# Kernel optimization log

Hardware: AMD Instinct MI355X
Metric: run time of the kernel (lower is better)

## Reference

```python
import jax, jax.numpy as jnp
import numpy as np

N_NODES = 100000
N_EDGES = 3200000
D_IN = 256
D_OUT = 256


def setup_inputs() -> dict:
    key = jax.random.key(0)
    k1, k2, k3, k4, k5 = jax.random.split(key, 5)
    inputs = jax.random.normal(k1, (N_NODES, D_IN), dtype=jnp.float32)
    # Glorot-uniform init as in _glorot_init
    init_range = np.sqrt(6.0 / (D_IN + D_OUT)).astype(np.float32)
    weight = jax.random.uniform(k2, (D_IN, D_OUT), dtype=jnp.float32,
                                minval=-init_range, maxval=init_range)
    edge_src = jax.random.randint(k3, (N_EDGES,), 0, N_NODES, dtype=jnp.int32)
    edge_dst = jax.random.randint(k4, (N_EDGES,), 0, N_NODES, dtype=jnp.int32)
    # normalized adjacency values (positive, like D^-1/2 A D^-1/2 entries)
    edge_vals = jax.random.uniform(k5, (N_EDGES,), dtype=jnp.float32)
    return {"inputs": inputs, "weight": weight, "edge_src": edge_src,
            "edge_dst": edge_dst, "edge_vals": edge_vals}


def reference(inputs, weight, edge_src, edge_dst, edge_vals):
    # x = inputs @ W          : [N, D_OUT]
    x = inputs @ weight
    # SpMM: out[d] = sum_{e: dst(e)=d} vals[e] * x[src(e)]
    msgs = edge_vals[:, None] * x[edge_src]          # [E, D_OUT]
    out = jax.ops.segment_sum(msgs, edge_dst, num_segments=inputs.shape[0])
    return jax.nn.relu(out)
```

## Files before the change

### kernel.cpp

```cpp
#include <hip/hip_runtime.h>

#define N_NODES 100000
#define N_EDGES 3200000
#define DDIM 256
#define NB 1563
#define BIN_BLK 256
#define CHUNK (N_EDGES / BIN_BLK)
#define TB 1024

typedef short s16x8 __attribute__((ext_vector_type(8)));
typedef float f32x4 __attribute__((ext_vector_type(4)));
typedef float f32x2 __attribute__((ext_vector_type(2)));

__device__ __forceinline__ unsigned short f32_to_bf16(float f) {
    union { float f; unsigned int u; } c; c.f = f;
    unsigned int u = c.u;
    unsigned int r = u + 0x7fffu + ((u >> 16) & 1u);
    return (unsigned short)(r >> 16);
}
__device__ __forceinline__ float bl16(unsigned int u) {
    union { unsigned int x; float f; } c; c.x = u << 16; return c.f;
}
__device__ __forceinline__ float bh16(unsigned int u) {
    union { unsigned int x; float f; } c; c.x = u & 0xffff0000u; return c.f;
}

__global__ __launch_bounds__(256) void prep_w(const float* __restrict__ W,
                                              unsigned short* __restrict__ Wt) {
    __shared__ float tile[32][33];
    const int tx = threadIdx.x & 31;
    const int ty = threadIdx.x >> 5;
    const int n0 = blockIdx.x * 32;
    const int k0 = blockIdx.y * 32;
    for (int i = 0; i < 32; i += 8)
        tile[ty + i][tx] = W[(size_t)(k0 + ty + i) * DDIM + n0 + tx];
    __syncthreads();
    for (int i = 0; i < 32; i += 8)
        Wt[(size_t)(n0 + ty + i) * DDIM + k0 + tx] = f32_to_bf16(tile[tx][ty + i]);
}

__global__ __launch_bounds__(256) void gemm_mfma(const float* __restrict__ A,
                                                 const unsigned short* __restrict__ Wt,
                                                 unsigned short* __restrict__ Xb) {
    __shared__ unsigned short As[64][DDIM + 8];
    const int tid = threadIdx.x;
    const int rowBase = blockIdx.x * 64;

#pragma unroll
    for (int p = 0; p < 16; ++p) {
        const int flat = p * 256 + tid;
        const int row = flat >> 6;
        const int k4 = (flat & 63) * 4;
        const int gr = rowBase + row;
        float4 v = make_float4(0.f, 0.f, 0.f, 0.f);
        if (gr < N_NODES) v = *(const float4*)&A[(size_t)gr * DDIM + k4];
        ushort4 h;
        h.x = f32_to_bf16(v.x); h.y = f32_to_bf16(v.y);
        h.z = f32_to_bf16(v.z); h.w = f32_to_bf16(v.w);
        *(ushort4*)&As[row][k4] = h;
    }
    __syncthreads();

    const int wave = tid >> 6;
    const int lane = tid & 63;
    const int lrow = lane & 15;
    const int quad = lane >> 4;
    const int cb = wave * 64;

    f32x4 acc[4][4] = {};

#pragma unroll
    for (int ks = 0; ks < 8; ++ks) {
        const int k0 = ks * 32 + quad * 8;
        s16x8 a[4], b[4];
#pragma unroll
        for (int ri = 0; ri < 4; ++ri)
            a[ri] = *(const s16x8*)&As[ri * 16 + lrow][k0];
#pragma unroll
        for (int ci = 0; ci < 4; ++ci)
            b[ci] = *(const s16x8*)&Wt[(size_t)(cb + ci * 16 + lrow) * DDIM + k0];
#pragma unroll
        for (int ri = 0; ri < 4; ++ri)
#pragma unroll
            for (int ci = 0; ci < 4; ++ci)
                acc[ri][ci] = __builtin_amdgcn_mfma_f32_16x16x32_bf16(a[ri], b[ci], acc[ri][ci], 0, 0, 0);
    }

#pragma unroll
    for (int ri = 0; ri < 4; ++ri) {
        const int r0 = rowBase + ri * 16 + quad * 4;
#pragma unroll
        for (int rr = 0; rr < 4; ++rr) {
            const int row = r0 + rr;
            if (row < N_NODES) {
#pragma unroll
                for (int ci = 0; ci < 4; ++ci)
                    Xb[(size_t)row * DDIM + cb + ci * 16 + lrow] = f32_to_bf16(acc[ri][ci][rr]);
            }
        }
    }
}

__global__ __launch_bounds__(TB) void hist_coarse(const int* __restrict__ edst,
                                                  int* __restrict__ gcounts) {
    __shared__ int h[NB];
    const int tid = threadIdx.x;
    for (int i = tid; i < NB; i += TB) h[i] = 0;
    __syncthreads();
    const int lo = blockIdx.x * CHUNK;
    const int hi = lo + CHUNK;
    for (int e = lo + tid; e < hi; e += TB) atomicAdd(&h[edst[e] >> 6], 1);
    __syncthreads();
    for (int i = tid; i < NB; i += TB)
        if (h[i]) atomicAdd(&gcounts[i], h[i]);
}

__global__ __launch_bounds__(256) void scan_coarse(const int* __restrict__ gcounts,
                                                   int* __restrict__ bbase,
                                                   int* __restrict__ bcursor,
                                                   int* __restrict__ off) {
    __shared__ int part[256];
    const int t = threadIdx.x;
    const int chunk = (NB + 255) / 256;
    const int lo = t * chunk;
    const int hi = min(lo + chunk, NB);
    int s = 0;
    for (int i = lo; i < hi; ++i) s += gcounts[i];
    part[t] = s;
    __syncthreads();
    for (int d = 1; d < 256; d <<= 1) {
        int a = (t >= d) ? part[t - d] : 0;
        __syncthreads();
        part[t] += a;
        __syncthreads();
    }
    int run = part[t] - s;
    for (int i = lo; i < hi; ++i) {
        bbase[i] = run;
        bcursor[i] = run;
        run += gcounts[i];
    }
    if (t == 255) {
        bbase[NB] = run;
        off[N_NODES] = run;
    }
}

__global__ __launch_bounds__(TB) void bin_coarse(const int* __restrict__ esrc,
                                                 const int* __restrict__ edst,
                                                 const float* __restrict__ evals,
                                                 int* __restrict__ bcursor,
                                                 long long* __restrict__ tmp) {
    __shared__ int h[NB];
    __shared__ int sb[NB];
    const int tid = threadIdx.x;
    for (int i = tid; i < NB; i += TB) h[i] = 0;
    __syncthreads();
    const int lo = blockIdx.x * CHUNK;
    const int hi = lo + CHUNK;
    for (int e = lo + tid; e < hi; e += TB) atomicAdd(&h[edst[e] >> 6], 1);
    __syncthreads();
    for (int i = tid; i < NB; i += TB)
        sb[i] = h[i] ? atomicAdd(&bcursor[i], h[i]) : 0;
    __syncthreads();
    for (int e = lo + tid; e < hi; e += TB) {
        const int d = edst[e];
        const int b = d >> 6;
        const int p = atomicAdd(&sb[b], 1);
        const unsigned int lo32 = (unsigned int)(esrc[e] | ((d & 63) << 17));
        const unsigned int hi32 = (unsigned int)__float_as_int(evals[e]);
        tmp[p] = (long long)(((unsigned long long)hi32 << 32) | lo32);
    }
}

__global__ __launch_bounds__(256) void refine(const long long* __restrict__ tmp,
                                              const int* __restrict__ bbase,
                                              int* __restrict__ off,
                                              long long* __restrict__ srcval) {
    __shared__ int nh[64];
    __shared__ int nb[64];
    const int b = blockIdx.x;
    const int tid = threadIdx.x;
    const int base = bbase[b];
    const int cnt = bbase[b + 1] - base;
    const int n0 = b * 64;
    const int nn = min(64, N_NODES - n0);
    if (tid < 64) nh[tid] = 0;
    __syncthreads();
    for (int i = tid; i < cnt; i += 256) {
        const long long q = tmp[base + i];
        atomicAdd(&nh[((int)(unsigned int)q) >> 17], 1);
    }
    __syncthreads();
    if (tid == 0) {
        int run = 0;
        for (int i = 0; i < 64; ++i) { nb[i] = run; run += nh[i]; }
    }
    __syncthreads();
    if (tid < nn) off[n0 + tid] = base + nb[tid];
    __syncthreads();
    for (int i = tid; i < cnt; i += 256) {
        const long long q = tmp[base + i];
        const unsigned int lo32 = (unsigned int)q;
        const int dl = (int)(lo32 >> 17);
        const int p = atomicAdd(&nb[dl], 1);
        srcval[base + p] = (long long)((q & 0xFFFFFFFF00000000ull) | (lo32 & 0x1FFFF));
    }
}

#define HEDGE(q) { a0 += v##q * bl16(h##q); a1 += v##q * bh16(h##q); }

__global__ __launch_bounds__(256) void spmm_half(const unsigned short* __restrict__ xbh,
                                                 const int* __restrict__ off,
                                                 const long long* __restrict__ srcval,
                                                 float* __restrict__ outh) {
    const int node = blockIdx.x * 4 + (threadIdx.x >> 6);
    const int lane = threadIdx.x & 63;
    const int start = off[node];
    const int end = off[node + 1];

    const unsigned short* xcol = xbh + lane * 2;
    float a0 = 0.f, a1 = 0.f;

    for (int base = start; base < end; base += 64) {
        const int cnt = min(64, end - base);
        int s_l = 0;
        float v_l = 0.f;
        if (lane < cnt) {
            const long long q = __builtin_nontemporal_load(&srcval[base + lane]);
            s_l = (int)((unsigned int)q & 0x1FFFF);
            v_l = __int_as_float((int)(q >> 32));
        }
        int j = 0;
        for (; j + 8 <= cnt; j += 8) {
            const int s0 = __shfl(s_l, j + 0);
            const int s1 = __shfl(s_l, j + 1);
            const int s2 = __shfl(s_l, j + 2);
            const int s3 = __shfl(s_l, j + 3);
            const int s4 = __shfl(s_l, j + 4);
            const int s5 = __shfl(s_l, j + 5);
            const int s6 = __shfl(s_l, j + 6);
            const int s7 = __shfl(s_l, j + 7);
            const float v0 = __shfl(v_l, j + 0);
            const float v1 = __shfl(v_l, j + 1);
            const float v2 = __shfl(v_l, j + 2);
            const float v3 = __shfl(v_l, j + 3);
            const float v4 = __shfl(v_l, j + 4);
            const float v5 = __shfl(v_l, j + 5);
            const float v6 = __shfl(v_l, j + 6);
            const float v7 = __shfl(v_l, j + 7);
            const unsigned int h0 = *(const unsigned int*)&xcol[(size_t)s0 * DDIM];
            const unsigned int h1 = *(const unsigned int*)&xcol[(size_t)s1 * DDIM];
            const unsigned int h2 = *(const unsigned int*)&xcol[(size_t)s2 * DDIM];
            const unsigned int h3 = *(const unsigned int*)&xcol[(size_t)s3 * DDIM];
            const unsigned int h4 = *(const unsigned int*)&xcol[(size_t)s4 * DDIM];
            const unsigned int h5 = *(const unsigned int*)&xcol[(size_t)s5 * DDIM];
            const unsigned int h6 = *(const unsigned int*)&xcol[(size_t)s6 * DDIM];
            const unsigned int h7 = *(const unsigned int*)&xcol[(size_t)s7 * DDIM];
            HEDGE(0) HEDGE(1) HEDGE(2) HEDGE(3)
            HEDGE(4) HEDGE(5) HEDGE(6) HEDGE(7)
        }
        for (; j < cnt; ++j) {
            const int s = __shfl(s_l, j);
            const float v = __shfl(v_l, j);
            const unsigned int h = *(const unsigned int*)&xcol[(size_t)s * DDIM];
            a0 += v * bl16(h); a1 += v * bh16(h);
        }
    }

    f32x2 o;
    o[0] = fmaxf(a0, 0.f);
    o[1] = fmaxf(a1, 0.f);
    __builtin_nontemporal_store(o, (f32x2*)&outh[(size_t)node * DDIM + lane * 2]);
}
#undef HEDGE

extern "C" void kernel_launch(void* const* d_in, const int* in_sizes, int n_in,
                              void* d_out, int out_size, void* d_ws, size_t ws_size,
                              hipStream_t stream) {
    const float* inputs = (const float*)d_in[0];
    const float* weight = (const float*)d_in[1];
    const int* esrc     = (const int*)d_in[2];
    const int* edst     = (const int*)d_in[3];
    const float* evals  = (const float*)d_in[4];
    float* out = (float*)d_out;

    unsigned short* xb = (unsigned short*)d_ws;
    unsigned short* Wt = xb + (size_t)N_NODES * DDIM;
    int* off     = (int*)(Wt + DDIM * DDIM);
    int* gcounts = off + N_NODES + 1;
    int* bbase   = gcounts + NB;
    int* bcursor = bbase + NB + 1;
    uintptr_t a  = ((uintptr_t)(bcursor + NB) + 15) & ~(uintptr_t)15;
    long long* tmp    = (long long*)a;
    long long* srcval = tmp + N_EDGES;

    prep_w<<<dim3(8, 8), 256, 0, stream>>>(weight, Wt);

    gemm_mfma<<<(N_NODES + 63) / 64, 256, 0, stream>>>(inputs, Wt, xb);

    (void)hipMemsetAsync(gcounts, 0, NB * sizeof(int), stream);
    hist_coarse<<<BIN_BLK, TB, 0, stream>>>(edst, gcounts);
    scan_coarse<<<1, 256, 0, stream>>>(gcounts, bbase, bcursor, off);
    bin_coarse<<<BIN_BLK, TB, 0, stream>>>(esrc, edst, evals, bcursor, tmp);
    refine<<<NB, 256, 0, stream>>>(tmp, bbase, off, srcval);

    spmm_half<<<N_NODES / 4, 256, 0, stream>>>(xb,       off, srcval, out);
    spmm_half<<<N_NODES / 4, 256, 0, stream>>>(xb + 128, off, srcval, out + 128);
}
```

Before: 561.3 us.

## Stage GEMM output through LDS, widen refine blocks, merge SpMM halves into one launch

The GEMM epilogue now writes bf16 results into shared memory and then stores them to global memory as coalesced 16-byte vectors, replacing scattered 2-byte stores. The refine kernel runs with 1024 threads per block instead of 256, which gives more parallelism per bucket. The two SpMM half launches become one launch with a 2-wide grid in y, which removes one launch and lets both halves run concurrently. Running the halves concurrently may reduce L2 locality for each half of X compared with processing them sequentially.

```diff
diff --git a/kernel.cpp b/kernel.cpp
--- a/kernel.cpp
+++ b/kernel.cpp
@@ -86,18 +86,25 @@
                 acc[ri][ci] = __builtin_amdgcn_mfma_f32_16x16x32_bf16(a[ri], b[ci], acc[ri][ci], 0, 0, 0);
     }
 
-#pragma unroll
-    for (int ri = 0; ri < 4; ++ri) {
-        const int r0 = rowBase + ri * 16 + quad * 4;
-#pragma unroll
-        for (int rr = 0; rr < 4; ++rr) {
-            const int row = r0 + rr;
-            if (row < N_NODES) {
-#pragma unroll
-                for (int ci = 0; ci < 4; ++ci)
-                    Xb[(size_t)row * DDIM + cb + ci * 16 + lrow] = f32_to_bf16(acc[ri][ci][rr]);
-            }
-        }
+    __syncthreads();
+#pragma unroll
+    for (int ri = 0; ri < 4; ++ri)
+#pragma unroll
+        for (int rr = 0; rr < 4; ++rr)
+#pragma unroll
+            for (int ci = 0; ci < 4; ++ci)
+                As[ri * 16 + quad * 4 + rr][cb + ci * 16 + lrow] =
+                    f32_to_bf16(acc[ri][ci][rr]);
+    __syncthreads();
+
+#pragma unroll
+    for (int it = 0; it < 8; ++it) {
+        const int flat = it * 256 + tid;
+        const int row  = flat >> 5;
+        const int c8   = (flat & 31) * 8;
+        const int grow = rowBase + row;
+        if (grow < N_NODES)
+            *(s16x8*)&Xb[(size_t)grow * DDIM + c8] = *(const s16x8*)&As[row][c8];
     }
 }
 
@@ -173,10 +180,10 @@
     }
 }
 
-__global__ __launch_bounds__(256) void refine(const long long* __restrict__ tmp,
-                                              const int* __restrict__ bbase,
-                                              int* __restrict__ off,
-                                              long long* __restrict__ srcval) {
+__global__ __launch_bounds__(TB) void refine(const long long* __restrict__ tmp,
+                                             const int* __restrict__ bbase,
+                                             int* __restrict__ off,
+                                             long long* __restrict__ srcval) {
     __shared__ int nh[64];
     __shared__ int nb[64];
     const int b = blockIdx.x;
@@ -187,7 +194,7 @@
     const int nn = min(64, N_NODES - n0);
     if (tid < 64) nh[tid] = 0;
     __syncthreads();
-    for (int i = tid; i < cnt; i += 256) {
+    for (int i = tid; i < cnt; i += TB) {
         const long long q = tmp[base + i];
         atomicAdd(&nh[((int)(unsigned int)q) >> 17], 1);
     }
@@ -199,7 +206,7 @@
     __syncthreads();
     if (tid < nn) off[n0 + tid] = base + nb[tid];
     __syncthreads();
-    for (int i = tid; i < cnt; i += 256) {
+    for (int i = tid; i < cnt; i += TB) {
         const long long q = tmp[base + i];
         const unsigned int lo32 = (unsigned int)q;
         const int dl = (int)(lo32 >> 17);
@@ -210,16 +217,17 @@
 
 #define HEDGE(q) { a0 += v##q * bl16(h##q); a1 += v##q * bh16(h##q); }
 
-__global__ __launch_bounds__(256) void spmm_half(const unsigned short* __restrict__ xbh,
+__global__ __launch_bounds__(256) void spmm_half(const unsigned short* __restrict__ xb,
                                                  const int* __restrict__ off,
                                                  const long long* __restrict__ srcval,
-                                                 float* __restrict__ outh) {
+                                                 float* __restrict__ out) {
     const int node = blockIdx.x * 4 + (threadIdx.x >> 6);
     const int lane = threadIdx.x & 63;
+    const int dimoff = blockIdx.y << 7;
     const int start = off[node];
     const int end = off[node + 1];
 
-    const unsigned short* xcol = xbh + lane * 2;
+    const unsigned short* xcol = xb + dimoff + lane * 2;
     float a0 = 0.f, a1 = 0.f;
 
     for (int base = start; base < end; base += 64) {
@@ -271,7 +279,7 @@
     f32x2 o;
     o[0] = fmaxf(a0, 0.f);
     o[1] = fmaxf(a1, 0.f);
-    __builtin_nontemporal_store(o, (f32x2*)&outh[(size_t)node * DDIM + lane * 2]);
+    __builtin_nontemporal_store(o, (f32x2*)&out[(size_t)node * DDIM + dimoff + lane * 2]);
 }
 #undef HEDGE
 
@@ -303,8 +311,7 @@
     hist_coarse<<<BIN_BLK, TB, 0, stream>>>(edst, gcounts);
     scan_coarse<<<1, 256, 0, stream>>>(gcounts, bbase, bcursor, off);
     bin_coarse<<<BIN_BLK, TB, 0, stream>>>(esrc, edst, evals, bcursor, tmp);
-    refine<<<NB, 256, 0, stream>>>(tmp, bbase, off, srcval);
-
-    spmm_half<<<N_NODES / 4, 256, 0, stream>>>(xb,       off, srcval, out);
-    spmm_half<<<N_NODES / 4, 256, 0, stream>>>(xb + 128, off, srcval, out + 128);
-}
+    refine<<<NB, TB, 0, stream>>>(tmp, bbase, off, srcval);
+
+    spmm_half<<<dim3(N_NODES / 4, 2), 256, 0, stream>>>(xb, off, srcval, out);
+}
```

Measured after the change: 548.3 us. 1.02x faster.
